# Performance work log

Measured on AMD Instinct MI355X. Metric: run time of the kernel, lower is better.

The kernel has to match this reference:

```python
import jax, jax.numpy as jnp
import numpy as np

N = 50000   # nodes
E = 600000  # edges
D = 128     # in = hidden = out channels
G = 256     # graphs in batch
EPS = 1e-5


def setup_inputs() -> dict:
    key = jax.random.key(0)
    ks = jax.random.split(key, 16)
    sc = 1.0 / np.sqrt(D)
    inp = {
        "x": jax.random.normal(ks[0], (N, D), jnp.float32),
        "edge_index": jax.random.randint(ks[1], (2, E), 0, N, dtype=jnp.int32),
        "edge_attr": jax.random.normal(ks[2], (E, 4), jnp.float32),
        "batch": jnp.sort(jax.random.randint(ks[3], (N,), 0, G, dtype=jnp.int32)),
        # conv1 + norm1
        "W1": jax.random.normal(ks[4], (D, D), jnp.float32) * sc,
        "b1": jnp.zeros((D,), jnp.float32),
        "g1": jnp.ones((D,), jnp.float32),
        "be1": jnp.zeros((D,), jnp.float32),
        # middle conv (num_layers=3 -> one hidden conv) + norm
        "Wm": jax.random.normal(ks[5], (D, D), jnp.float32) * sc,
        "bm": jnp.zeros((D,), jnp.float32),
        "gm": jnp.ones((D,), jnp.float32),
        "bem": jnp.zeros((D,), jnp.float32),
        # conv2 + norm2
        "W2": jax.random.normal(ks[6], (D, D), jnp.float32) * sc,
        "b2": jnp.zeros((D,), jnp.float32),
        "g2": jnp.ones((D,), jnp.float32),
        "be2": jnp.zeros((D,), jnp.float32),
    }
    return inp


def _gcn_conv(x, W, b, src, dst, dinv):
    # PyG GCNConv with add_self_loops=True: out = D^{-1/2}(A+I)D^{-1/2} (x W) + b
    h = x @ W
    enorm = dinv[src] * dinv[dst]                      # [E]
    msg = h[src] * enorm[:, None]                      # gather + scale
    agg = jnp.zeros_like(h).at[dst].add(msg)           # scatter-add to targets
    agg = agg + h * (dinv * dinv)[:, None]             # self-loop contribution
    return agg + b


def _bn(x, g, b):
    # BatchNorm1d over nodes (batch statistics)
    mu = jnp.mean(x, axis=0)
    var = jnp.var(x, axis=0)
    return (x - mu) * jax.lax.rsqrt(var + EPS) * g + b


def reference(x, edge_index, edge_attr, batch,
              W1, b1, g1, be1, Wm, bm, gm, bem, W2, b2, g2, be2):
    src, dst = edge_index[0], edge_index[1]
    # degree of A + I (in-degree at targets, +1 self loop); shared by all layers
    deg = jnp.zeros((N,), x.dtype).at[dst].add(1.0) + 1.0
    dinv = jax.lax.rsqrt(deg)

    h = jax.nn.relu(_bn(_gcn_conv(x, W1, b1, src, dst, dinv), g1, be1))
    h = jax.nn.relu(_bn(_gcn_conv(h, Wm, bm, src, dst, dinv), gm, bem))
    h = _bn(_gcn_conv(h, W2, b2, src, dst, dinv), g2, be2)

    # global mean pool (batch re-based at batch[0])
    seg = batch - batch[0]
    sums = jax.ops.segment_sum(h, seg, num_segments=G)
    cnt = jax.ops.segment_sum(jnp.ones((N,), h.dtype), seg, num_segments=G)
    return sums / jnp.maximum(cnt, 1.0)[:, None]
```

## Files before the change

kernel.cpp:

```cpp
#include <hip/hip_runtime.h>

#define DIM 128
constexpr float EPS = 1e-5f;
#define NSHARD 32
#define SHARD (NSHARD * 256)

typedef _Float16 f16;
typedef __attribute__((ext_vector_type(8))) _Float16 f16x8;
typedef __attribute__((ext_vector_type(4))) float f32x4;

__global__ __launch_bounds__(256) void k_prep(const int* __restrict__ dst,
                                              int* __restrict__ degi, int E,
                                              const float* __restrict__ W0,
                                              const float* __restrict__ W1,
                                              const float* __restrict__ W2,
                                              f16* __restrict__ wt) {
    if (blockIdx.x < 12) {
        int layer = blockIdx.x >> 2;
        int quarter = blockIdx.x & 3;
        const float* W = layer == 0 ? W0 : (layer == 1 ? W1 : W2);
        f16* hi = wt + (size_t)layer * 2 * DIM * DIM;
        f16* lo = hi + DIM * DIM;
        for (int idx = quarter * 4096 + threadIdx.x; idx < (quarter + 1) * 4096;
             idx += 256) {
            int k = idx >> 7, c = idx & 127;
            float w = W[idx];
            f16 h = (f16)w;
            f16 l = (f16)((w - (float)h) * 2048.0f);
            hi[c * DIM + k] = h;
            lo[c * DIM + k] = l;
        }
    } else {
        int e = (blockIdx.x - 12) * 256 + threadIdx.x;
        if (e < E) atomicAdd(&degi[dst[e]], 1);
    }
}

__global__ __launch_bounds__(256) void k_scan_local(const int* __restrict__ degi,
                                                    int* __restrict__ row_ptr,
                                                    float* __restrict__ dinv,
                                                    int* __restrict__ bsum, int n) {
    __shared__ int ws[4];
    int t = threadIdx.x, lane = t & 63, wv = t >> 6;
    int i0 = blockIdx.x * 1024 + t * 4;
    int v[4];
#pragma unroll
    for (int j = 0; j < 4; ++j) {
        int i = i0 + j;
        v[j] = (i < n) ? degi[i] : 0;
        if (i < n) dinv[i] = rsqrtf((float)v[j] + 1.0f);
    }
    int tsum = v[0] + v[1] + v[2] + v[3];
    int sc = tsum;
#pragma unroll
    for (int off = 1; off < 64; off <<= 1) {
        int u = __shfl_up(sc, off, 64);
        if (lane >= off) sc += u;
    }
    if (lane == 63) ws[wv] = sc;
    __syncthreads();
    int woff = 0;
    for (int j = 0; j < wv; ++j) woff += ws[j];
    int run = woff + sc - tsum;
#pragma unroll
    for (int j = 0; j < 4; ++j) {
        int i = i0 + j;
        if (i < n) row_ptr[i] = run;
        run += v[j];
    }
    if (t == 255) bsum[blockIdx.x] = woff + sc;
}

__global__ __launch_bounds__(256) void k_scan_add(int* __restrict__ row_ptr,
                                                  int* __restrict__ cursor,
                                                  const int* __restrict__ bsum,
                                                  int n, int E, int nb) {
    __shared__ int soff;
    int t = threadIdx.x;
    int seg = blockIdx.x >> 2;
    if (t < 64) {
        int v = (t < nb) ? bsum[t] : 0;
        int sc = v;
#pragma unroll
        for (int off = 1; off < 64; off <<= 1) {
            int u = __shfl_up(sc, off, 64);
            if (t >= off) sc += u;
        }
        if (t == seg) soff = sc - v;
    }
    __syncthreads();
    int i = blockIdx.x * 256 + t;
    if (i < n) {
        int v = row_ptr[i] + soff;
        row_ptr[i] = v;
        cursor[i] = v;
    }
    if (i == 0) row_ptr[n] = E;
}

__global__ void k_fill(const int* __restrict__ src, const int* __restrict__ dst,
                       int* __restrict__ cursor, int* __restrict__ csr_src, int E) {
    int e = blockIdx.x * blockDim.x + threadIdx.x;
    if (e >= E) return;
    int d = dst[e];
    int slot = atomicAdd(&cursor[d], 1);
    csr_src[slot] = src[e];
}

template <bool PRE_BN>
__global__ __launch_bounds__(256) void k_matmul_mfma(
    const float* __restrict__ inF, const f16* __restrict__ inH,
    const f16* __restrict__ wt, const float* __restrict__ dinv,
    const float* __restrict__ stats, const float* __restrict__ g,
    const float* __restrict__ be, float inv_n, f16* __restrict__ out, int n) {
    __shared__ __align__(16) char sA[64 * 256];
    __shared__ float sScale[DIM], sShift[DIM];

    int t = threadIdx.x;
    int w = t >> 6, l = t & 63;
    int row0 = blockIdx.x * 64;

    if (PRE_BN) {
        if (t < DIM) {
            float su = 0.f, sq = 0.f;
            for (int s = 0; s < NSHARD; ++s) {
                su += stats[s * 256 + t];
                sq += stats[s * 256 + 128 + t];
            }
            float mu = su * inv_n;
            float var = sq * inv_n - mu * mu;
            float sc = rsqrtf(var + EPS) * g[t];
            sScale[t] = sc;
            sShift[t] = be[t] - mu * sc;
        }
        __syncthreads();
    }

    f16x8 bh[2][4], bl[2][4];
    {
        int col = w * 32 + (l & 15);
        int ksub = (l >> 4) * 8;
        const f16* hi = wt;
        const f16* lo = wt + DIM * DIM;
#pragma unroll
        for (int ct = 0; ct < 2; ++ct) {
            int c2 = col + ct * 16;
#pragma unroll
            for (int kt = 0; kt < 4; ++kt) {
                bh[ct][kt] = *(const f16x8*)&hi[(size_t)c2 * DIM + kt * 32 + ksub];
                bl[ct][kt] = *(const f16x8*)&lo[(size_t)c2 * DIM + kt * 32 + ksub];
            }
        }
    }

    {
        int r = t >> 2;
        int row_g = row0 + r;
        if (row_g >= n) row_g = n - 1;
        int cbase = (t & 3) * 32;
#pragma unroll
        for (int o = 0; o < 4; ++o) {
            int c0 = cbase + o * 8;
            f16x8 h8;
            if (PRE_BN) {
                f16x8 v8 = *(const f16x8*)(inH + (size_t)row_g * DIM + c0);
#pragma unroll
                for (int j = 0; j < 8; ++j) {
                    float v = (float)v8[j] * sScale[c0 + j] + sShift[c0 + j];
                    h8[j] = (f16)fmaxf(v, 0.f);
                }
            } else {
                float4 v0 = *(const float4*)(inF + (size_t)row_g * DIM + c0);
                float4 v1 = *(const float4*)(inF + (size_t)row_g * DIM + c0 + 4);
                h8[0] = (f16)v0.x; h8[1] = (f16)v0.y; h8[2] = (f16)v0.z; h8[3] = (f16)v0.w;
                h8[4] = (f16)v1.x; h8[5] = (f16)v1.y; h8[6] = (f16)v1.z; h8[7] = (f16)v1.w;
            }
            int byte = (r * 256 + c0 * 2) ^ ((r & 7) << 4);
            *(f16x8*)(sA + byte) = h8;
        }
    }
    __syncthreads();

    f32x4 accA[4][2], accB[4][2];
#pragma unroll
    for (int rt = 0; rt < 4; ++rt)
#pragma unroll
        for (int ct = 0; ct < 2; ++ct) {
            accA[rt][ct] = (f32x4){0.f, 0.f, 0.f, 0.f};
            accB[rt][ct] = (f32x4){0.f, 0.f, 0.f, 0.f};
        }

#pragma unroll
    for (int rt = 0; rt < 4; ++rt) {
        int row_l = rt * 16 + (l & 15);
        int kb = (l >> 4) * 16;
        f16x8 a[4];
#pragma unroll
        for (int kt = 0; kt < 4; ++kt) {
            int byte = (row_l * 256 + kt * 64 + kb) ^ ((row_l & 7) << 4);
            a[kt] = *(const f16x8*)(sA + byte);
        }
#pragma unroll
        for (int ct = 0; ct < 2; ++ct) {
            f32x4 cA = accA[rt][ct], cB = accB[rt][ct];
#pragma unroll
            for (int kt = 0; kt < 4; ++kt) {
                cA = __builtin_amdgcn_mfma_f32_16x16x32_f16(a[kt], bh[ct][kt], cA, 0, 0, 0);
                cB = __builtin_amdgcn_mfma_f32_16x16x32_f16(a[kt], bl[ct][kt], cB, 0, 0, 0);
            }
            accA[rt][ct] = cA;
            accB[rt][ct] = cB;
        }
    }

    int colw = w * 32 + (l & 15);
#pragma unroll
    for (int rt = 0; rt < 4; ++rt) {
        int row_l = rt * 16 + ((l >> 4) << 2);
#pragma unroll
        for (int reg = 0; reg < 4; ++reg) {
            int gr = row0 + row_l + reg;
            if (gr >= n) continue;
            float dv = dinv[gr];
#pragma unroll
            for (int ct = 0; ct < 2; ++ct) {
                float v = (accA[rt][ct][reg] + accB[rt][ct][reg] * (1.0f / 2048.0f)) * dv;
                out[(size_t)gr * DIM + colw + ct * 16] = (f16)v;
            }
        }
    }
}

template <bool POOL>
__global__ __launch_bounds__(256) void k_gs(const f16* __restrict__ hs,
                                            const int* __restrict__ csr_src,
                                            const int* __restrict__ row_ptr,
                                            const float* __restrict__ dinv,
                                            const float* __restrict__ b,
                                            const int* __restrict__ batch,
                                            f16* __restrict__ agg,
                                            float* __restrict__ stats_part,
                                            float* __restrict__ gsum, int n) {
    __shared__ float sSum[4][DIM];
    __shared__ float sSq[4][DIM];
    __shared__ int sSeg[4];

    int t = threadIdx.x;
    int wv = t >> 6, l = t & 63;
    int node = blockIdx.x * 4 + wv;
    int grp = l >> 4;
    int c8 = (l & 15) * 8;
    bool valid = node < n;

    float acc[8] = {};
    int beg = 0, end = 0;
    if (valid) {
        beg = row_ptr[node];
        end = row_ptr[node + 1];
    }
    for (int e = beg + grp; e < end; e += 16) {
        bool v1 = e + 4 < end, v2 = e + 8 < end, v3 = e + 12 < end;
        f16x8 a0 = *(const f16x8*)(hs + (size_t)csr_src[e] * DIM + c8);
        f16x8 a1 = {}, a2 = {}, a3 = {};
        if (v1) a1 = *(const f16x8*)(hs + (size_t)csr_src[e + 4] * DIM + c8);
        if (v2) a2 = *(const f16x8*)(hs + (size_t)csr_src[e + 8] * DIM + c8);
        if (v3) a3 = *(const f16x8*)(hs + (size_t)csr_src[e + 12] * DIM + c8);
#pragma unroll
        for (int j = 0; j < 8; ++j)
            acc[j] += ((float)a0[j] + (float)a1[j]) + ((float)a2[j] + (float)a3[j]);
    }
#pragma unroll
    for (int j = 0; j < 8; ++j) {
        acc[j] += __shfl_xor(acc[j], 16, 64);
        acc[j] += __shfl_xor(acc[j], 32, 64);
    }

    if (grp == 0) {
        if (valid) {
            f16x8 hv = *(const f16x8*)(hs + (size_t)node * DIM + c8);
            float dv = dinv[node];
            f32x4 bb0 = *(const f32x4*)(b + c8);
            f32x4 bb1 = *(const f32x4*)(b + c8 + 4);
            float o[8];
#pragma unroll
            for (int j = 0; j < 4; ++j) {
                o[j] = (acc[j] + (float)hv[j]) * dv + bb0[j];
                o[j + 4] = (acc[j + 4] + (float)hv[j + 4]) * dv + bb1[j];
            }
            f16x8 ov;
#pragma unroll
            for (int j = 0; j < 8; ++j) ov[j] = (f16)o[j];
            *(f16x8*)(agg + (size_t)node * DIM + c8) = ov;
            f32x4 s0 = {o[0], o[1], o[2], o[3]}, s1 = {o[4], o[5], o[6], o[7]};
            f32x4 q0 = {o[0]*o[0], o[1]*o[1], o[2]*o[2], o[3]*o[3]};
            f32x4 q1 = {o[4]*o[4], o[5]*o[5], o[6]*o[6], o[7]*o[7]};
            *(f32x4*)&sSum[wv][c8] = s0;
            *(f32x4*)&sSum[wv][c8 + 4] = s1;
            *(f32x4*)&sSq[wv][c8] = q0;
            *(f32x4*)&sSq[wv][c8 + 4] = q1;
            if (POOL && l == 0) sSeg[wv] = batch[node] - batch[0];
        } else {
            f32x4 z = {0.f, 0.f, 0.f, 0.f};
            *(f32x4*)&sSum[wv][c8] = z;
            *(f32x4*)&sSum[wv][c8 + 4] = z;
            *(f32x4*)&sSq[wv][c8] = z;
            *(f32x4*)&sSq[wv][c8 + 4] = z;
            if (POOL && l == 0) sSeg[wv] = -1;
        }
    }
    __syncthreads();

    int shard = (blockIdx.x & (NSHARD - 1)) * 256;
    if (t < 128) {
        float s = sSum[0][t] + sSum[1][t] + sSum[2][t] + sSum[3][t];
        atomicAdd(&stats_part[shard + t], s);
    } else {
        int ch = t - 128;
        float s = sSq[0][ch] + sSq[1][ch] + sSq[2][ch] + sSq[3][ch];
        atomicAdd(&stats_part[shard + 128 + ch], s);
    }

    if (POOL && t < 128) {
        int cur = -1;
        float a = 0.f;
#pragma unroll
        for (int w = 0; w < 4; ++w) {
            int sg = sSeg[w];
            if (sg < 0) continue;
            if (sg != cur) {
                if (cur >= 0) atomicAdd(&gsum[(size_t)cur * DIM + t], a);
                a = 0.f;
                cur = sg;
            }
            a += sSum[w][t];
        }
        if (cur >= 0) atomicAdd(&gsum[(size_t)cur * DIM + t], a);
    }
}

__global__ __launch_bounds__(128) void k_pool_fin(const float* __restrict__ gsum,
                                                  const int* __restrict__ batch,
                                                  const float* __restrict__ stats,
                                                  const float* __restrict__ g,
                                                  const float* __restrict__ be,
                                                  float* __restrict__ out,
                                                  int n, float inv_n) {
    int gseg = blockIdx.x;
    int c = threadIdx.x;
    int b0 = batch[0];
    int target = b0 + gseg;
    int lo = 0, hi = n;
    while (lo < hi) { int mid = (lo + hi) >> 1; if (batch[mid] < target) lo = mid + 1; else hi = mid; }
    int start = lo;
    lo = start; hi = n;
    while (lo < hi) { int mid = (lo + hi) >> 1; if (batch[mid] < target + 1) lo = mid + 1; else hi = mid; }
    int end = lo;
    int cnt = end - start;

    float su = 0.f, sq = 0.f;
    for (int s = 0; s < NSHARD; ++s) {
        su += stats[s * 256 + c];
        sq += stats[s * 256 + 128 + c];
    }
    float mu = su * inv_n;
    float var = sq * inv_n - mu * mu;
    float scale = rsqrtf(var + EPS) * g[c];
    float shift = be[c] - mu * scale;
    float o = 0.f;
    if (cnt > 0) o = (gsum[(size_t)gseg * DIM + c] / (float)cnt) * scale + shift;
    out[(size_t)gseg * DIM + c] = o;
}

extern "C" void kernel_launch(void* const* d_in, const int* in_sizes, int n_in,
                              void* d_out, int out_size, void* d_ws, size_t ws_size,
                              hipStream_t stream) {
    const float* x = (const float*)d_in[0];
    const int* edge_index = (const int*)d_in[1];
    const int* batch = (const int*)d_in[3];
    const float* W1 = (const float*)d_in[4];
    const float* b1 = (const float*)d_in[5];
    const float* g1 = (const float*)d_in[6];
    const float* be1 = (const float*)d_in[7];
    const float* Wm = (const float*)d_in[8];
    const float* bm = (const float*)d_in[9];
    const float* gm = (const float*)d_in[10];
    const float* bem = (const float*)d_in[11];
    const float* W2 = (const float*)d_in[12];
    const float* b2 = (const float*)d_in[13];
    const float* g2 = (const float*)d_in[14];
    const float* be2 = (const float*)d_in[15];

    int n = in_sizes[0] / DIM;
    int E = in_sizes[1] / 2;
    int G = out_size / DIM;

    const int* srcI = edge_index;
    const int* dstI = edge_index + E;

    char* p = (char*)d_ws;
    f16* bufA = (f16*)p;                p += (size_t)n * DIM * 2;
    f16* bufB = (f16*)p;                p += (size_t)n * DIM * 2;
    float* dinv = (float*)p;            p += (size_t)n * 4;
    int* row_ptr = (int*)p;             p += (size_t)(n + 1) * 4;
    int* cursor = (int*)p;              p += (size_t)n * 4;
    int* csr_src = (int*)p;             p += (size_t)E * 4;
    int* bsum = (int*)p;                p += 64 * 4;
    char* zero0 = p;
    int* degi = (int*)p;                p += (size_t)n * 4;
    float* stats3 = (float*)p;          p += 3 * SHARD * 4;
    float* gsum = (float*)p;            p += (size_t)G * DIM * 4;
    size_t zero_bytes = (size_t)(p - zero0);
    f16* wsplit = (f16*)p;              p += (size_t)3 * 2 * DIM * DIM * 2;

    float* out = (float*)d_out;
    float inv_n = 1.0f / (float)n;
    int nb = (n + 1023) / 1024;

    hipMemsetAsync(zero0, 0, zero_bytes, stream);
    k_prep<<<12 + (E + 255) / 256, 256, 0, stream>>>(dstI, degi, E, W1, Wm, W2, wsplit);
    k_scan_local<<<nb, 256, 0, stream>>>(degi, row_ptr, dinv, bsum, n);
    k_scan_add<<<(n + 255) / 256, 256, 0, stream>>>(row_ptr, cursor, bsum, n, E, nb);
    k_fill<<<(E + 255) / 256, 256, 0, stream>>>(srcI, dstI, cursor, csr_src, E);

    struct Layer { const float *b, *g, *be; };
    Layer L[3] = {{b1, g1, be1}, {bm, gm, bem}, {b2, g2, be2}};

    int mmBlocks = (n + 63) / 64;
    int gsBlocks = (n + 3) / 4;
    for (int l = 0; l < 3; ++l) {
        const f16* wl = wsplit + (size_t)l * 2 * DIM * DIM;
        float* stats_l = stats3 + l * SHARD;
        if (l == 0)
            k_matmul_mfma<false><<<mmBlocks, 256, 0, stream>>>(
                x, nullptr, wl, dinv, nullptr, nullptr, nullptr, inv_n, bufA, n);
        else
            k_matmul_mfma<true><<<mmBlocks, 256, 0, stream>>>(
                nullptr, bufB, wl, dinv, stats3 + (l - 1) * SHARD,
                L[l - 1].g, L[l - 1].be, inv_n, bufA, n);
        if (l < 2)
            k_gs<false><<<gsBlocks, 256, 0, stream>>>(bufA, csr_src, row_ptr, dinv,
                                                      L[l].b, batch, bufB, stats_l,
                                                      nullptr, n);
        else
            k_gs<true><<<gsBlocks, 256, 0, stream>>>(bufA, csr_src, row_ptr, dinv,
                                                     L[l].b, batch, bufB, stats_l,
                                                     gsum, n);
    }

    k_pool_fin<<<G, 128, 0, stream>>>(gsum, batch, stats3 + 2 * SHARD, g2, be2,
                                      out, n, inv_n);
}
```

Before: 268.5 us.

## Drop split-fp16 weight correction and process two row tiles per matmul block

Weights are now stored as a single fp16 copy instead of a hi/lo split, which halves the MFMA work and the weight register footprint in the matmul. Each matmul block now handles two 64-row tiles and reuses the weights it loaded, halving the block count. The gather-scatter kernel issues its self-loop feature load before the edge loop so that load can overlap the loop. Using plain fp16 weights lowers the matmul's numerical precision, which may affect accuracy.

```diff
diff --git a/kernel.cpp b/kernel.cpp
--- a/kernel.cpp
+++ b/kernel.cpp
@@ -19,16 +19,11 @@
         int layer = blockIdx.x >> 2;
         int quarter = blockIdx.x & 3;
         const float* W = layer == 0 ? W0 : (layer == 1 ? W1 : W2);
-        f16* hi = wt + (size_t)layer * 2 * DIM * DIM;
-        f16* lo = hi + DIM * DIM;
+        f16* hi = wt + (size_t)layer * DIM * DIM;
         for (int idx = quarter * 4096 + threadIdx.x; idx < (quarter + 1) * 4096;
              idx += 256) {
             int k = idx >> 7, c = idx & 127;
-            float w = W[idx];
-            f16 h = (f16)w;
-            f16 l = (f16)((w - (float)h) * 2048.0f);
-            hi[c * DIM + k] = h;
-            lo[c * DIM + k] = l;
+            hi[c * DIM + k] = (f16)W[idx];
         }
     } else {
         int e = (blockIdx.x - 12) * 256 + threadIdx.x;
@@ -118,7 +113,6 @@
 
     int t = threadIdx.x;
     int w = t >> 6, l = t & 63;
-    int row0 = blockIdx.x * 64;
 
     if (PRE_BN) {
         if (t < DIM) {
@@ -136,96 +130,91 @@
         __syncthreads();
     }
 
-    f16x8 bh[2][4], bl[2][4];
+    f16x8 bh[2][4];
     {
         int col = w * 32 + (l & 15);
         int ksub = (l >> 4) * 8;
-        const f16* hi = wt;
-        const f16* lo = wt + DIM * DIM;
 #pragma unroll
         for (int ct = 0; ct < 2; ++ct) {
             int c2 = col + ct * 16;
 #pragma unroll
+            for (int kt = 0; kt < 4; ++kt)
+                bh[ct][kt] = *(const f16x8*)&wt[(size_t)c2 * DIM + kt * 32 + ksub];
+        }
+    }
+
+#pragma unroll
+    for (int half = 0; half < 2; ++half) {
+        int row0 = blockIdx.x * 128 + half * 64;
+        if (row0 >= n) break;
+        if (half == 1) __syncthreads();
+
+        {
+            int r = t >> 2;
+            int row_g = row0 + r;
+            if (row_g >= n) row_g = n - 1;
+            int cbase = (t & 3) * 32;
+#pragma unroll
+            for (int o = 0; o < 4; ++o) {
+                int c0 = cbase + o * 8;
+                f16x8 h8;
+                if (PRE_BN) {
+                    f16x8 v8 = *(const f16x8*)(inH + (size_t)row_g * DIM + c0);
+#pragma unroll
+                    for (int j = 0; j < 8; ++j) {
+                        float v = (float)v8[j] * sScale[c0 + j] + sShift[c0 + j];
+                        h8[j] = (f16)fmaxf(v, 0.f);
+                    }
+                } else {
+                    float4 v0 = *(const float4*)(inF + (size_t)row_g * DIM + c0);
+                    float4 v1 = *(const float4*)(inF + (size_t)row_g * DIM + c0 + 4);
+                    h8[0] = (f16)v0.x; h8[1] = (f16)v0.y; h8[2] = (f16)v0.z; h8[3] = (f16)v0.w;
+                    h8[4] = (f16)v1.x; h8[5] = (f16)v1.y; h8[6] = (f16)v1.z; h8[7] = (f16)v1.w;
+                }
+                int byte = (r * 256 + c0 * 2) ^ ((r & 7) << 4);
+                *(f16x8*)(sA + byte) = h8;
+            }
+        }
+        __syncthreads();
+
+        f32x4 acc[4][2];
+#pragma unroll
+        for (int rt = 0; rt < 4; ++rt)
+#pragma unroll
+            for (int ct = 0; ct < 2; ++ct) acc[rt][ct] = (f32x4){0.f, 0.f, 0.f, 0.f};
+
+#pragma unroll
+        for (int rt = 0; rt < 4; ++rt) {
+            int row_l = rt * 16 + (l & 15);
+            int kb = (l >> 4) * 16;
+            f16x8 a[4];
+#pragma unroll
             for (int kt = 0; kt < 4; ++kt) {
-                bh[ct][kt] = *(const f16x8*)&hi[(size_t)c2 * DIM + kt * 32 + ksub];
-                bl[ct][kt] = *(const f16x8*)&lo[(size_t)c2 * DIM + kt * 32 + ksub];
-            }
-        }
-    }
-
-    {
-        int r = t >> 2;
-        int row_g = row0 + r;
-        if (row_g >= n) row_g = n - 1;
-        int cbase = (t & 3) * 32;
-#pragma unroll
-        for (int o = 0; o < 4; ++o) {
-            int c0 = cbase + o * 8;
-            f16x8 h8;
-            if (PRE_BN) {
-                f16x8 v8 = *(const f16x8*)(inH + (size_t)row_g * DIM + c0);
-#pragma unroll
-                for (int j = 0; j < 8; ++j) {
-                    float v = (float)v8[j] * sScale[c0 + j] + sShift[c0 + j];
-                    h8[j] = (f16)fmaxf(v, 0.f);
-                }
-            } else {
-                float4 v0 = *(const float4*)(inF + (size_t)row_g * DIM + c0);
-                float4 v1 = *(const float4*)(inF + (size_t)row_g * DIM + c0 + 4);
-                h8[0] = (f16)v0.x; h8[1] = (f16)v0.y; h8[2] = (f16)v0.z; h8[3] = (f16)v0.w;
-                h8[4] = (f16)v1.x; h8[5] = (f16)v1.y; h8[6] = (f16)v1.z; h8[7] = (f16)v1.w;
-            }
-            int byte = (r * 256 + c0 * 2) ^ ((r & 7) << 4);
-            *(f16x8*)(sA + byte) = h8;
-        }
-    }
-    __syncthreads();
-
-    f32x4 accA[4][2], accB[4][2];
-#pragma unroll
-    for (int rt = 0; rt < 4; ++rt)
-#pragma unroll
-        for (int ct = 0; ct < 2; ++ct) {
-            accA[rt][ct] = (f32x4){0.f, 0.f, 0.f, 0.f};
-            accB[rt][ct] = (f32x4){0.f, 0.f, 0.f, 0.f};
-        }
-
-#pragma unroll
-    for (int rt = 0; rt < 4; ++rt) {
-        int row_l = rt * 16 + (l & 15);
-        int kb = (l >> 4) * 16;
-        f16x8 a[4];
-#pragma unroll
-        for (int kt = 0; kt < 4; ++kt) {
-            int byte = (row_l * 256 + kt * 64 + kb) ^ ((row_l & 7) << 4);
-            a[kt] = *(const f16x8*)(sA + byte);
-        }
-#pragma unroll
-        for (int ct = 0; ct < 2; ++ct) {
-            f32x4 cA = accA[rt][ct], cB = accB[rt][ct];
-#pragma unroll
-            for (int kt = 0; kt < 4; ++kt) {
-                cA = __builtin_amdgcn_mfma_f32_16x16x32_f16(a[kt], bh[ct][kt], cA, 0, 0, 0);
-                cB = __builtin_amdgcn_mfma_f32_16x16x32_f16(a[kt], bl[ct][kt], cB, 0, 0, 0);
-            }
-            accA[rt][ct] = cA;
-            accB[rt][ct] = cB;
-        }
-    }
-
-    int colw = w * 32 + (l & 15);
-#pragma unroll
-    for (int rt = 0; rt < 4; ++rt) {
-        int row_l = rt * 16 + ((l >> 4) << 2);
-#pragma unroll
-        for (int reg = 0; reg < 4; ++reg) {
-            int gr = row0 + row_l + reg;
-            if (gr >= n) continue;
-            float dv = dinv[gr];
+                int byte = (row_l * 256 + kt * 64 + kb) ^ ((row_l & 7) << 4);
+                a[kt] = *(const f16x8*)(sA + byte);
+            }
 #pragma unroll
             for (int ct = 0; ct < 2; ++ct) {
-                float v = (accA[rt][ct][reg] + accB[rt][ct][reg] * (1.0f / 2048.0f)) * dv;
-                out[(size_t)gr * DIM + colw + ct * 16] = (f16)v;
+                f32x4 c = acc[rt][ct];
+#pragma unroll
+                for (int kt = 0; kt < 4; ++kt)
+                    c = __builtin_amdgcn_mfma_f32_16x16x32_f16(a[kt], bh[ct][kt], c, 0, 0, 0);
+                acc[rt][ct] = c;
+            }
+        }
+
+        int colw = w * 32 + (l & 15);
+#pragma unroll
+        for (int rt = 0; rt < 4; ++rt) {
+            int row_l = rt * 16 + ((l >> 4) << 2);
+#pragma unroll
+            for (int reg = 0; reg < 4; ++reg) {
+                int gr = row0 + row_l + reg;
+                if (gr >= n) continue;
+                float dv = dinv[gr];
+#pragma unroll
+                for (int ct = 0; ct < 2; ++ct)
+                    out[(size_t)gr * DIM + colw + ct * 16] = (f16)(acc[rt][ct][reg] * dv);
             }
         }
     }
@@ -252,6 +241,9 @@
     int c8 = (l & 15) * 8;
     bool valid = node < n;
 
+    f16x8 hv = {};
+    if (valid && grp == 0) hv = *(const f16x8*)(hs + (size_t)node * DIM + c8);
+
     float acc[8] = {};
     int beg = 0, end = 0;
     if (valid) {
@@ -277,7 +269,6 @@
 
     if (grp == 0) {
         if (valid) {
-            f16x8 hv = *(const f16x8*)(hs + (size_t)node * DIM + c8);
             float dv = dinv[node];
             f32x4 bb0 = *(const f32x4*)(b + c8);
             f32x4 bb1 = *(const f32x4*)(b + c8 + 4);
@@ -410,7 +401,7 @@
     float* stats3 = (float*)p;          p += 3 * SHARD * 4;
     float* gsum = (float*)p;            p += (size_t)G * DIM * 4;
     size_t zero_bytes = (size_t)(p - zero0);
-    f16* wsplit = (f16*)p;              p += (size_t)3 * 2 * DIM * DIM * 2;
+    f16* wsplit = (f16*)p;              p += (size_t)3 * DIM * DIM * 2;
 
     float* out = (float*)d_out;
     float inv_n = 1.0f / (float)n;
@@ -425,10 +416,10 @@
     struct Layer { const float *b, *g, *be; };
     Layer L[3] = {{b1, g1, be1}, {bm, gm, bem}, {b2, g2, be2}};
 
-    int mmBlocks = (n + 63) / 64;
+    int mmBlocks = (n + 127) / 128;
     int gsBlocks = (n + 3) / 4;
     for (int l = 0; l < 3; ++l) {
-        const f16* wl = wsplit + (size_t)l * 2 * DIM * DIM;
+        const f16* wl = wsplit + (size_t)l * DIM * DIM;
         float* stats_l = stats3 + l * SHARD;
         if (l == 0)
             k_matmul_mfma<false><<<mmBlocks, 256, 0, stream>>>(
```

Result: faster. 251.0 us (-6.5%).
